# Optimization experiments

Measured on AMD Instinct MI355X. Metric: run time of the kernel, lower is better.

Reference implementation:

```python
import jax, jax.numpy as jnp
import numpy as np

B, T, D = 2, 1024, 1024
NUM_HEADS_ARG = 16
HS = D // NUM_HEADS_ARG          # 64 (per-head size)
H = HS                           # bug in source: num_heads passed = head_size -> 64 heads
FF = 4 * D
EPS = 1e-5


def _layernorm(x, gamma, beta):
    mu = jnp.mean(x, axis=-1, keepdims=True)
    var = jnp.mean(jnp.square(x - mu), axis=-1, keepdims=True)
    return (x - mu) * jax.lax.rsqrt(var + EPS) * gamma + beta


def setup_inputs() -> dict:
    key = jax.random.key(0)
    ks = jax.random.split(key, 12)
    s_d = 1.0 / np.sqrt(D)
    s_cat = 1.0 / np.sqrt(H * HS)
    s_ff = 1.0 / np.sqrt(FF)
    return {
        "x": jax.random.normal(ks[0], (B, T, D), jnp.float32),
        "Wq": jax.random.uniform(ks[1], (H, D, HS), jnp.float32, -s_d, s_d),
        "Wk": jax.random.uniform(ks[2], (H, D, HS), jnp.float32, -s_d, s_d),
        "Wv": jax.random.uniform(ks[3], (H, D, HS), jnp.float32, -s_d, s_d),
        "Wo": jax.random.uniform(ks[4], (H * HS, D), jnp.float32, -s_cat, s_cat),
        "bo": jax.random.uniform(ks[5], (D,), jnp.float32, -s_cat, s_cat),
        "W1": jax.random.uniform(ks[6], (D, FF), jnp.float32, -s_d, s_d),
        "b1": jax.random.uniform(ks[7], (FF,), jnp.float32, -s_d, s_d),
        "W2": jax.random.uniform(ks[8], (FF, D), jnp.float32, -s_ff, s_ff),
        "b2": jax.random.uniform(ks[9], (D,), jnp.float32, -s_ff, s_ff),
        "g1": jnp.ones((D,), jnp.float32),
        "be1": jnp.zeros((D,), jnp.float32),
        "g2": jnp.ones((D,), jnp.float32),
        "be2": jnp.zeros((D,), jnp.float32),
    }


def reference(x, Wq, Wk, Wv, Wo, bo, W1, b1, W2, b2, g1, be1, g2, be2):
    # per-head projections (no bias): [B,H,T,hs]
    q = jnp.einsum('btd,hde->bhte', x, Wq)
    k = jnp.einsum('btd,hde->bhte', x, Wk)
    v = jnp.einsum('btd,hde->bhte', x, Wv)
    scores = jnp.einsum('bhte,bhse->bhts', q, k) / np.sqrt(HS)  # [B,H,T,T]
    causal = jnp.tril(jnp.ones((T, T), bool))
    scores = jnp.where(causal, scores, -jnp.inf)
    probs = jax.nn.softmax(scores, axis=-1)
    att = jnp.einsum('bhts,bhse->bhte', probs, v)               # [B,H,T,hs]
    # torch stack(dim=3) -> [B,T,hs,H] then flatten: index = d*H + h
    cat = jnp.transpose(att, (0, 2, 3, 1)).reshape(B, T, HS * H)
    mha = cat @ Wo + bo
    x1 = _layernorm(x + mha, g1, be1)
    ff = jax.nn.relu(x1 @ W1 + b1) @ W2 + b2
    return _layernorm(x1 + ff, g2, be2)
```

## Files before the change

### kernel.cpp

```cpp
#include <hip/hip_runtime.h>

typedef unsigned short u16;
typedef __bf16 bf16x8 __attribute__((ext_vector_type(8)));
typedef float f32x4 __attribute__((ext_vector_type(4)));

#define B_ 2
#define T_ 1024
#define D_ 1024
#define H_ 64
#define HS_ 64
#define FF_ 4096
#define SZ_QKV 8388608L
#define S_SCALE 0.1803368801111f

__device__ __forceinline__ float bf2f(u16 u) {
  union { unsigned int v; float f; } x; x.v = ((unsigned int)u) << 16; return x.f;
}
__device__ __forceinline__ u16 f2bf(float f) {
  union { float f; unsigned int v; } x; x.f = f;
  unsigned int r = x.v + 0x7fffu + ((x.v >> 16) & 1u);
  return (u16)(r >> 16);
}
__device__ __forceinline__ u16 f2bf_rtz(float f) {
  union { float f; unsigned int v; } x; x.f = f;
  return (u16)(x.v >> 16);
}

typedef __attribute__((address_space(3))) unsigned int lds_u32;
typedef __attribute__((address_space(1))) const unsigned int glb_u32;
__device__ __forceinline__ void gload_lds16(const void* g, void* l) {
  __builtin_amdgcn_global_load_lds((glb_u32*)g, (lds_u32*)l, 16, 0, 0);
}

__global__ __launch_bounds__(256) void prep(
    const float* __restrict__ x, const float* __restrict__ Wq,
    const float* __restrict__ Wk, const float* __restrict__ Wv,
    const float* __restrict__ Wo, const float* __restrict__ W1,
    const float* __restrict__ W2,
    u16* __restrict__ xb, u16* __restrict__ Wqkvt, u16* __restrict__ Wot,
    u16* __restrict__ W1t, u16* __restrict__ W2t)
{
  __shared__ float tile[64][65];
  int id = blockIdx.x;
  if (id < 1024) {
    const long i = ((long)id * 256 + threadIdx.x) * 8;
    float4 a = *(const float4*)(x + i);
    float4 b = *(const float4*)(x + i + 4);
    union { uint4 v; u16 u[8]; } o;
    o.u[0]=f2bf(a.x); o.u[1]=f2bf(a.y); o.u[2]=f2bf(a.z); o.u[3]=f2bf(a.w);
    o.u[4]=f2bf(b.x); o.u[5]=f2bf(b.y); o.u[6]=f2bf(b.z); o.u[7]=f2bf(b.w);
    *(uint4*)(xb + i) = o.v;
    return;
  }
  id -= 1024;
  const float* in; u16* out; long ibase, obase; int in_rs, out_rs, r0, c0;
  if (id < 3072) {
    const int w = id >> 10, rem = id & 1023;
    const int z = rem >> 4, rt = rem & 15;
    in = (w == 0) ? Wq : (w == 1) ? Wk : Wv;
    ibase = (long)z * 65536; in_rs = 64; r0 = rt * 64; c0 = 0;
    out = Wqkvt + (long)w * 4194304;
    obase = (long)z * 65536; out_rs = 1024;
  } else if (id < 4096) {
    const int rem = id - 3072;
    const int z = rem >> 4, ct = rem & 15;
    in = Wo; ibase = (long)z * 1024; in_rs = 65536; r0 = 0; c0 = ct * 64;
    out = Wot; obase = (long)z * 64; out_rs = 4096;
  } else if (id < 5120) {
    const int rem = id - 4096;
    const int rt = rem >> 6, ct = rem & 63;
    in = W1; ibase = 0; in_rs = 4096; r0 = rt * 64; c0 = ct * 64;
    out = W1t; obase = 0; out_rs = 1024;
  } else {
    const int rem = id - 5120;
    const int rt = rem >> 4, ct = rem & 15;
    in = W2; ibase = 0; in_rs = 1024; r0 = rt * 64; c0 = ct * 64;
    out = W2t; obase = 0; out_rs = 4096;
  }
  const int t = threadIdx.x, lr = t >> 4, lc4 = (t & 15) * 4;
  #pragma unroll
  for (int j = 0; j < 4; ++j) {
    float4 f = *(const float4*)(in + ibase + (long)(r0 + lr + j * 16) * in_rs + c0 + lc4);
    tile[lr + j * 16][lc4]     = f.x;
    tile[lr + j * 16][lc4 + 1] = f.y;
    tile[lr + j * 16][lc4 + 2] = f.z;
    tile[lr + j * 16][lc4 + 3] = f.w;
  }
  __syncthreads();
  const int cr = t >> 3, ch = t & 7;
  #pragma unroll
  for (int j2 = 0; j2 < 2; ++j2) {
    const int crr = cr + j2 * 32;
    union { uint4 v; u16 u[8]; } o;
    #pragma unroll
    for (int i = 0; i < 8; ++i) o.u[i] = f2bf(tile[ch * 8 + i][crr]);
    *(uint4*)(out + obase + (long)(c0 + crr) * out_rs + r0 + ch * 8) = o.v;
  }
}

template<int EPI, int LDA, int LDB>
__global__ __launch_bounds__(256, 2) void gemm2(
    const u16* __restrict__ A, const u16* __restrict__ Bt, u16* __restrict__ C,
    const float* __restrict__ bias, int K, int koff, int ldc)
{
  __shared__ __attribute__((aligned(16))) u16 As[3][256 * 32];
  __shared__ __attribute__((aligned(16))) u16 Bs[3][128 * 32];
  const int bm = blockIdx.x, bn = blockIdx.y, bz = blockIdx.z;
  const long ko = (long)bz * koff;
  const int tid = threadIdx.x, wave = tid >> 6, lane = tid & 63;
  const int quad = lane >> 4, l16 = lane & 15;
  const int wm = (wave & 1) * 128;
  const int wn = (wave >> 1) * 64;
  const int srcswz = ((lane & 3) ^ ((lane >> 3) & 3)) * 8;
  const int arr = lane >> 2;
  const int cs8 = (quad ^ ((l16 >> 1) & 3)) * 8;
  const u16* Arow = A + (long)(bm * 256) * LDA + ko + srcswz;
  const u16* Brow = Bt + (long)(bn * 128) * LDB + ko + srcswz;

  f32x4 acc[8][4];
  #pragma unroll
  for (int i = 0; i < 8; ++i)
    #pragma unroll
    for (int j = 0; j < 4; ++j) acc[i][j] = (f32x4){0.f, 0.f, 0.f, 0.f};

  const int nK = K >> 5;

  auto STAGE = [&](int buf, int t) {
    const int k0 = t << 5;
    #pragma unroll
    for (int it = 0; it < 4; ++it) {
      const int i = it * 4 + wave;
      gload_lds16(Arow + (long)(i * 16 + arr) * LDA + k0, (u16*)As[buf] + i * 512);
    }
    #pragma unroll
    for (int it = 0; it < 2; ++it) {
      const int i = it * 4 + wave;
      gload_lds16(Brow + (long)(i * 16 + arr) * LDB + k0, (u16*)Bs[buf] + i * 512);
    }
  };

  STAGE(0, 0);
  STAGE(1, 1);
  int cc = 0, cs = 2;
  for (int t = 0; t < nK; ++t) {
    if (t < nK - 1) asm volatile("s_waitcnt vmcnt(6)" ::: "memory");
    else            asm volatile("s_waitcnt vmcnt(0)" ::: "memory");
    __builtin_amdgcn_sched_barrier(0);
    __builtin_amdgcn_s_barrier();
    __builtin_amdgcn_sched_barrier(0);
    if (t + 2 < nK) STAGE(cs, t + 2);
    const u16* At = As[cc];
    const u16* Bl = Bs[cc];
    bf16x8 a[8], b[4];
    #pragma unroll
    for (int j = 0; j < 4; ++j)
      b[j] = *(const bf16x8*)&Bl[(wn + j * 16 + l16) * 32 + cs8];
    #pragma unroll
    for (int i = 0; i < 8; ++i)
      a[i] = *(const bf16x8*)&At[(wm + i * 16 + l16) * 32 + cs8];
    #pragma unroll
    for (int i = 0; i < 8; ++i)
      #pragma unroll
      for (int j = 0; j < 4; ++j)
        acc[i][j] = __builtin_amdgcn_mfma_f32_16x16x32_bf16(a[i], b[j], acc[i][j], 0, 0, 0);
    cc = (cc == 2) ? 0 : cc + 1;
    cs = (cs == 2) ? 0 : cs + 1;
  }

  #pragma unroll
  for (int j = 0; j < 4; ++j) {
    const int col = bn * 128 + wn + j * 16 + l16;
    const float bval = (EPI == 1) ? bias[col] : 0.f;
    #pragma unroll
    for (int i = 0; i < 8; ++i) {
      #pragma unroll
      for (int r = 0; r < 4; ++r) {
        const int row = bm * 256 + wm + i * 16 + quad * 4 + r;
        float vv = acc[i][j][r] + bval;
        if (EPI == 1) vv = fmaxf(vv, 0.f);
        if (EPI == 2) {
          const int which = col >> 12, rem = col & 4095;
          const int h = rem >> 6, e = rem & 63;
          const int bb = row >> 10, t = row & 1023;
          C[(long)which * SZ_QKV + ((long)((bb << 6) + h)) * 65536L + t * 64 + e] = f2bf(vv);
        } else if (EPI == 3) {
          ((float*)C)[(long)bz * 2097152 + (long)row * ldc + col] = vv;
        } else {
          C[(long)row * ldc + col] = f2bf(vv);
        }
      }
    }
  }
}

__global__ __launch_bounds__(256) void attn_flash(
    const u16* __restrict__ Q, const u16* __restrict__ Kg,
    const u16* __restrict__ V, u16* __restrict__ Om)
{
  __shared__ __attribute__((aligned(16))) u16 Ks[2][64][72];
  __shared__ __attribute__((aligned(16))) u16 Vs[2][64][72];
  __shared__ __attribute__((aligned(16))) u16 QP[4][16][72];
  const int bh = blockIdx.x;
  const int qt = gridDim.y - 1 - blockIdx.y;
  const int b = bh >> 6, h = bh & 63;
  const long base = (long)bh * (T_ * HS_);
  const int tid = threadIdx.x;
  const int wave = tid >> 6, lane = tid & 63, quad = lane >> 4, l16 = lane & 15;
  const int sm = tid >> 2, sc = (tid & 3) * 16;
  const int vswz = (sc >> 4) << 3;

  {
    const int qr = lane >> 3, qe = (lane & 7) * 8;
    #pragma unroll
    for (int j = 0; j < 2; ++j) {
      union { uint4 v; u16 u[8]; } a, o;
      a.v = *(const uint4*)(Q + base + (long)(qt * 64 + wave * 16 + qr + j * 8) * HS_ + qe);
      #pragma unroll
      for (int i = 0; i < 8; ++i) o.u[i] = f2bf(bf2f(a.u[i]) * S_SCALE);
      *(uint4*)&QP[wave][qr + j * 8][qe] = o.v;
    }
  }
  bf16x8 aq0 = *(const bf16x8*)&QP[wave][l16][quad * 8];
  bf16x8 aq1 = *(const bf16x8*)&QP[wave][l16][32 + quad * 8];

  float psum[4] = { 0.f, 0.f, 0.f, 0.f };
  f32x4 oacc[4] = { {0,0,0,0}, {0,0,0,0}, {0,0,0,0}, {0,0,0,0} };

  uint4 kA, kB, vA, vB;
  kA = *(const uint4*)(Kg + base + (long)sm * HS_ + sc);
  kB = *(const uint4*)(Kg + base + (long)sm * HS_ + sc + 8);
  vA = *(const uint4*)(V  + base + (long)sm * HS_ + sc);
  vB = *(const uint4*)(V  + base + (long)sm * HS_ + sc + 8);
  {
    *(uint4*)&Ks[0][sm][sc] = kA; *(uint4*)&Ks[0][sm][sc + 8] = kB;
    union { uint4 v; u16 u[8]; } t0, t1; t0.v = vA; t1.v = vB;
    #pragma unroll
    for (int i = 0; i < 8; ++i) Vs[0][sc + i][sm ^ vswz] = t0.u[i];
    #pragma unroll
    for (int i = 0; i < 8; ++i) Vs[0][sc + 8 + i][sm ^ vswz] = t1.u[i];
  }
  __syncthreads();

  for (int kt = 0; kt <= qt; ++kt) {
    const int cur = kt & 1;
    const bool pf = (kt < qt);
    if (pf) {
      const long nb = base + (long)((kt + 1) * 64 + sm) * HS_ + sc;
      kA = *(const uint4*)(Kg + nb); kB = *(const uint4*)(Kg + nb + 8);
      vA = *(const uint4*)(V  + nb); vB = *(const uint4*)(V  + nb + 8);
    }

    f32x4 sacc[4] = { {0,0,0,0}, {0,0,0,0}, {0,0,0,0}, {0,0,0,0} };
    #pragma unroll
    for (int nt = 0; nt < 4; ++nt) {
      bf16x8 b0 = *(const bf16x8*)&Ks[cur][nt * 16 + l16][quad * 8];
      bf16x8 b1 = *(const bf16x8*)&Ks[cur][nt * 16 + l16][32 + quad * 8];
      sacc[nt] = __builtin_amdgcn_mfma_f32_16x16x32_bf16(aq0, b0, sacc[nt], 0, 0, 0);
      sacc[nt] = __builtin_amdgcn_mfma_f32_16x16x32_bf16(aq1, b1, sacc[nt], 0, 0, 0);
    }

    if (kt == qt) {
      #pragma unroll
      for (int nt = 0; nt < 4; ++nt) {
        const int col = nt * 16 + l16;
        #pragma unroll
        for (int r = 0; r < 4; ++r) {
          const int row = wave * 16 + quad * 4 + r;
          float p = exp2f(sacc[nt][r]);
          p = (col <= row) ? p : 0.f;
          sacc[nt][r] = p; psum[r] += p;
        }
      }
    } else {
      #pragma unroll
      for (int nt = 0; nt < 4; ++nt)
        #pragma unroll
        for (int r = 0; r < 4; ++r) {
          const float p = exp2f(sacc[nt][r]);
          sacc[nt][r] = p; psum[r] += p;
        }
    }

    #pragma unroll
    for (int nt = 0; nt < 4; ++nt)
      #pragma unroll
      for (int r = 0; r < 4; ++r)
        QP[wave][quad * 4 + r][nt * 16 + l16] = f2bf_rtz(sacc[nt][r]);
    bf16x8 p0 = *(const bf16x8*)&QP[wave][l16][quad * 8];
    bf16x8 p1 = *(const bf16x8*)&QP[wave][l16][32 + quad * 8];

    #pragma unroll
    for (int et = 0; et < 4; ++et) {
      const int c0 = ((quad ^ et) * 8);
      bf16x8 b0 = *(const bf16x8*)&Vs[cur][et * 16 + l16][c0];
      bf16x8 b1 = *(const bf16x8*)&Vs[cur][et * 16 + l16][32 + c0];
      oacc[et] = __builtin_amdgcn_mfma_f32_16x16x32_bf16(p0, b0, oacc[et], 0, 0, 0);
      oacc[et] = __builtin_amdgcn_mfma_f32_16x16x32_bf16(p1, b1, oacc[et], 0, 0, 0);
    }

    if (pf) {
      const int nxt = 1 - cur;
      *(uint4*)&Ks[nxt][sm][sc] = kA; *(uint4*)&Ks[nxt][sm][sc + 8] = kB;
      union { uint4 v; u16 u[8]; } t0, t1; t0.v = vA; t1.v = vB;
      #pragma unroll
      for (int i = 0; i < 8; ++i) Vs[nxt][sc + i][sm ^ vswz] = t0.u[i];
      #pragma unroll
      for (int i = 0; i < 8; ++i) Vs[nxt][sc + 8 + i][sm ^ vswz] = t1.u[i];
    }
    __syncthreads();
  }

  #pragma unroll
  for (int off = 1; off < 16; off <<= 1)
    #pragma unroll
    for (int r = 0; r < 4; ++r)
      psum[r] += __shfl_xor(psum[r], off, 64);
  u16 (*Os)[72] = Ks[0];
  #pragma unroll
  for (int r = 0; r < 4; ++r) {
    const float rinv = 1.f / fmaxf(psum[r], 1e-20f);
    const int row = wave * 16 + quad * 4 + r;
    #pragma unroll
    for (int et = 0; et < 4; ++et)
      Os[row][et * 16 + l16] = f2bf(oacc[et][r] * rinv);
  }
  const int orow = wave * 16 + (lane >> 3), oe = (lane & 7) * 8;
  #pragma unroll
  for (int it = 0; it < 2; ++it) {
    const int rr = orow + it * 8;
    uint4 o = *(const uint4*)&Os[rr][oe];
    *(uint4*)(Om + ((long)(b * T_ + qt * 64 + rr)) * 4096 + h * 64 + oe) = o;
  }
}

template<int XBF, int OBF>
__global__ __launch_bounds__(256) void ln_sum4(
    const float* __restrict__ P4, const float* __restrict__ bias,
    const void* __restrict__ Xv, const float* __restrict__ g,
    const float* __restrict__ be, void* __restrict__ outv)
{
  __shared__ float red[8];
  const int row = blockIdx.x, tid = threadIdx.x;
  const long base = (long)row * D_;
  float v4[4]; float s = 0.f;
  #pragma unroll
  for (int j = 0; j < 4; ++j) {
    const int i = tid + j * 256;
    float acc = bias[i];
    #pragma unroll
    for (int p = 0; p < 4; ++p) acc += P4[(long)p * 2097152 + base + i];
    const float xval = XBF ? bf2f(((const u16*)Xv)[base + i]) : ((const float*)Xv)[base + i];
    v4[j] = xval + acc;
    s += v4[j];
  }
  #pragma unroll
  for (int off = 32; off > 0; off >>= 1) s += __shfl_down(s, off, 64);
  if ((tid & 63) == 0) red[tid >> 6] = s;
  __syncthreads();
  const float mu = (red[0] + red[1] + red[2] + red[3]) * (1.f / D_);
  float vs = 0.f;
  #pragma unroll
  for (int j = 0; j < 4; ++j) { const float d = v4[j] - mu; vs += d * d; }
  #pragma unroll
  for (int off = 32; off > 0; off >>= 1) vs += __shfl_down(vs, off, 64);
  __syncthreads();
  if ((tid & 63) == 0) red[tid >> 6] = vs;
  __syncthreads();
  const float rs = rsqrtf((red[0] + red[1] + red[2] + red[3]) * (1.f / D_) + 1e-5f);
  #pragma unroll
  for (int j = 0; j < 4; ++j) {
    const int i = tid + j * 256;
    const float o = (v4[j] - mu) * rs * g[i] + be[i];
    if (OBF) ((u16*)outv)[base + i] = f2bf(o);
    else     ((float*)outv)[base + i] = o;
  }
}

extern "C" void kernel_launch(void* const* d_in, const int* in_sizes, int n_in,
                              void* d_out, int out_size, void* d_ws, size_t ws_size,
                              hipStream_t stream) {
  const float* x   = (const float*)d_in[0];
  const float* Wq  = (const float*)d_in[1];
  const float* Wk  = (const float*)d_in[2];
  const float* Wv  = (const float*)d_in[3];
  const float* Wo  = (const float*)d_in[4];
  const float* bo  = (const float*)d_in[5];
  const float* W1  = (const float*)d_in[6];
  const float* b1  = (const float*)d_in[7];
  const float* W2  = (const float*)d_in[8];
  const float* b2  = (const float*)d_in[9];
  const float* g1  = (const float*)d_in[10];
  const float* be1 = (const float*)d_in[11];
  const float* g2  = (const float*)d_in[12];
  const float* be2 = (const float*)d_in[13];
  float* out = (float*)d_out;

  u16* ws = (u16*)d_ws;
  u16* xb    = ws;
  u16* Wqkvt = xb + 2097152;
  u16* Wot   = Wqkvt + 12582912;
  u16* W1t   = Wot + 4194304;
  u16* W2t   = W1t + 4194304;
  u16* q     = W2t + 4194304;
  u16* k     = q + SZ_QKV;
  u16* v     = k + SZ_QKV;
  u16* Om    = v + SZ_QKV;
  float* P1 = (float*)q;
  float* P2 = (float*)q;
  u16* x1  = v;
  u16* h1  = Om;

  dim3 blk(256);

  prep<<<dim3(7168), blk, 0, stream>>>(x, Wq, Wk, Wv, Wo, W1, W2,
                                       xb, Wqkvt, Wot, W1t, W2t);

  gemm2<2, 1024, 1024><<<dim3(8, 96), blk, 0, stream>>>(
      xb, Wqkvt, q, nullptr, 1024, 0, 0);

  attn_flash<<<dim3(128, 16), blk, 0, stream>>>(q, k, v, Om);

  gemm2<3, 4096, 4096><<<dim3(8, 8, 4), blk, 0, stream>>>(
      Om, Wot, (u16*)P1, nullptr, 1024, 1024, 1024);

  ln_sum4<0, 1><<<dim3(2048), blk, 0, stream>>>(P1, bo, x, g1, be1, x1);

  gemm2<1, 1024, 1024><<<dim3(8, 32), blk, 0, stream>>>(
      x1, W1t, h1, b1, 1024, 0, 4096);

  gemm2<3, 4096, 4096><<<dim3(8, 8, 4), blk, 0, stream>>>(
      h1, W2t, (u16*)P2, nullptr, 1024, 1024, 1024);

  ln_sum4<1, 0><<<dim3(2048), blk, 0, stream>>>(P2, b2, x1, g2, be2, out);

  (void)in_sizes; (void)n_in; (void)out_size; (void)ws_size;
}
```

Before: 405.6 us.

## Replace 4-wave GEMM with 8-wave interleaved load/MFMA pipeline, K-tile 64

Replaces the 256-thread GEMM with a 512-thread kernel in which each of 8 waves computes a 64x64 sub-tile, and the K-step doubles to 64 with an XOR-swizzled LDS layout. Each K iteration is split into four quarter-phases. In each phase, LDS fragment loads and staged global-to-LDS copies for tile t+2 are interleaved with MFMA bursts under s_setprio and barriers, so memory traffic overlaps compute. The three-buffer LDS footprint grows to about 147KB, which allows only one block per CU. The extra barriers per iteration add synchronisation cost.

Result: faster. 387.9 us (-4.4%).

```diff
diff --git a/kernel.cpp b/kernel.cpp
--- a/kernel.cpp
+++ b/kernel.cpp
@@ -99,72 +99,148 @@
 }
 
 template<int EPI, int LDA, int LDB>
-__global__ __launch_bounds__(256, 2) void gemm2(
+__global__ __launch_bounds__(512, 2) void gemm8(
     const u16* __restrict__ A, const u16* __restrict__ Bt, u16* __restrict__ C,
     const float* __restrict__ bias, int K, int koff, int ldc)
 {
-  __shared__ __attribute__((aligned(16))) u16 As[3][256 * 32];
-  __shared__ __attribute__((aligned(16))) u16 Bs[3][128 * 32];
+  __shared__ __attribute__((aligned(16))) u16 As[3][256 * 64];
+  __shared__ __attribute__((aligned(16))) u16 Bs[3][128 * 64];
   const int bm = blockIdx.x, bn = blockIdx.y, bz = blockIdx.z;
   const long ko = (long)bz * koff;
   const int tid = threadIdx.x, wave = tid >> 6, lane = tid & 63;
   const int quad = lane >> 4, l16 = lane & 15;
-  const int wm = (wave & 1) * 128;
-  const int wn = (wave >> 1) * 64;
-  const int srcswz = ((lane & 3) ^ ((lane >> 3) & 3)) * 8;
-  const int arr = lane >> 2;
-  const int cs8 = (quad ^ ((l16 >> 1) & 3)) * 8;
-  const u16* Arow = A + (long)(bm * 256) * LDA + ko + srcswz;
-  const u16* Brow = Bt + (long)(bn * 128) * LDB + ko + srcswz;
-
-  f32x4 acc[8][4];
-  #pragma unroll
-  for (int i = 0; i < 8; ++i)
+  const int wm = (wave >> 1) * 64;
+  const int wn = (wave & 1) * 64;
+  const int slog = ((tid & 7) ^ ((tid >> 3) & 7)) * 8;
+  const int srow = tid >> 3;
+  const int ph0 = ((quad)     ^ (l16 & 7)) * 8;
+  const int ph1 = ((4 + quad) ^ (l16 & 7)) * 8;
+
+  const u16* Ag = A + (long)(bm * 256) * LDA + ko + slog;
+  const u16* Bg = Bt + (long)(bn * 128) * LDB + ko + slog;
+
+  f32x4 acc[4][4];
+  #pragma unroll
+  for (int i = 0; i < 4; ++i)
     #pragma unroll
     for (int j = 0; j < 4; ++j) acc[i][j] = (f32x4){0.f, 0.f, 0.f, 0.f};
 
-  const int nK = K >> 5;
-
-  auto STAGE = [&](int buf, int t) {
-    const int k0 = t << 5;
-    #pragma unroll
-    for (int it = 0; it < 4; ++it) {
-      const int i = it * 4 + wave;
-      gload_lds16(Arow + (long)(i * 16 + arr) * LDA + k0, (u16*)As[buf] + i * 512);
-    }
-    #pragma unroll
-    for (int it = 0; it < 2; ++it) {
-      const int i = it * 4 + wave;
-      gload_lds16(Brow + (long)(i * 16 + arr) * LDB + k0, (u16*)Bs[buf] + i * 512);
-    }
+  const int nK = K >> 6;
+
+  auto STAGE_A = [&](int d, int t, int half) {
+    const int kk = t << 6;
+    gload_lds16(Ag + (long)(half * 128 + srow) * LDA + kk,
+                (u16*)As[d] + (half * 1024 + tid) * 8);
+    gload_lds16(Ag + (long)(half * 128 + 64 + srow) * LDA + kk,
+                (u16*)As[d] + (half * 1024 + 512 + tid) * 8);
   };
-
-  STAGE(0, 0);
-  STAGE(1, 1);
-  int cc = 0, cs = 2;
+  auto STAGE_B = [&](int d, int t) {
+    const int kk = t << 6;
+    gload_lds16(Bg + (long)(srow) * LDB + kk, (u16*)Bs[d] + tid * 8);
+    gload_lds16(Bg + (long)(64 + srow) * LDB + kk, (u16*)Bs[d] + (512 + tid) * 8);
+  };
+
+  STAGE_A(0, 0, 0); STAGE_A(0, 0, 1); STAGE_B(0, 0);
+  STAGE_A(1, 1, 0); STAGE_A(1, 1, 1); STAGE_B(1, 1);
+
+  bf16x8 a0[2][2], b0[2][2], b1[2][2];
+  int cur = 0;
   for (int t = 0; t < nK; ++t) {
-    if (t < nK - 1) asm volatile("s_waitcnt vmcnt(6)" ::: "memory");
-    else            asm volatile("s_waitcnt vmcnt(0)" ::: "memory");
-    __builtin_amdgcn_sched_barrier(0);
-    __builtin_amdgcn_s_barrier();
-    __builtin_amdgcn_sched_barrier(0);
-    if (t + 2 < nK) STAGE(cs, t + 2);
-    const u16* At = As[cc];
-    const u16* Bl = Bs[cc];
-    bf16x8 a[8], b[4];
-    #pragma unroll
-    for (int j = 0; j < 4; ++j)
-      b[j] = *(const bf16x8*)&Bl[(wn + j * 16 + l16) * 32 + cs8];
-    #pragma unroll
-    for (int i = 0; i < 8; ++i)
-      a[i] = *(const bf16x8*)&At[(wm + i * 16 + l16) * 32 + cs8];
-    #pragma unroll
-    for (int i = 0; i < 8; ++i)
-      #pragma unroll
-      for (int j = 0; j < 4; ++j)
-        acc[i][j] = __builtin_amdgcn_mfma_f32_16x16x32_bf16(a[i], b[j], acc[i][j], 0, 0, 0);
-    cc = (cc == 2) ? 0 : cc + 1;
-    cs = (cs == 2) ? 0 : cs + 1;
+    const int nxt = (cur >= 1) ? cur - 1 : cur + 2;
+    const bool st = (t + 2) < nK;
+    const u16* Ab = As[cur];
+    const u16* Bb = Bs[cur];
+
+    if (t < nK - 1) { asm volatile("s_waitcnt vmcnt(6)" ::: "memory"); }
+    else            { asm volatile("s_waitcnt vmcnt(0)" ::: "memory"); }
+    __builtin_amdgcn_sched_barrier(0);
+    __builtin_amdgcn_s_barrier();
+    __builtin_amdgcn_sched_barrier(0);
+    #pragma unroll
+    for (int ii = 0; ii < 2; ++ii) {
+      const u16* r = Ab + (wm + ii * 16 + l16) * 64;
+      a0[ii][0] = *(const bf16x8*)(r + ph0);
+      a0[ii][1] = *(const bf16x8*)(r + ph1);
+    }
+    #pragma unroll
+    for (int jj = 0; jj < 2; ++jj) {
+      const u16* r = Bb + (wn + jj * 16 + l16) * 64;
+      b0[jj][0] = *(const bf16x8*)(r + ph0);
+      b0[jj][1] = *(const bf16x8*)(r + ph1);
+    }
+    asm volatile("s_waitcnt lgkmcnt(0)" ::: "memory");
+    __builtin_amdgcn_sched_barrier(0);
+    __builtin_amdgcn_s_setprio(1);
+    #pragma unroll
+    for (int ii = 0; ii < 2; ++ii)
+      #pragma unroll
+      for (int jj = 0; jj < 2; ++jj) {
+        acc[ii][jj] = __builtin_amdgcn_mfma_f32_16x16x32_bf16(a0[ii][0], b0[jj][0], acc[ii][jj], 0, 0, 0);
+        acc[ii][jj] = __builtin_amdgcn_mfma_f32_16x16x32_bf16(a0[ii][1], b0[jj][1], acc[ii][jj], 0, 0, 0);
+      }
+    __builtin_amdgcn_s_setprio(0);
+    __builtin_amdgcn_sched_barrier(0);
+    __builtin_amdgcn_s_barrier();
+
+    #pragma unroll
+    for (int jj = 0; jj < 2; ++jj) {
+      const u16* r = Bb + (wn + (2 + jj) * 16 + l16) * 64;
+      b1[jj][0] = *(const bf16x8*)(r + ph0);
+      b1[jj][1] = *(const bf16x8*)(r + ph1);
+    }
+    if (st) STAGE_A(nxt, t + 2, 0);
+    __builtin_amdgcn_s_barrier();
+    asm volatile("s_waitcnt lgkmcnt(0)" ::: "memory");
+    __builtin_amdgcn_sched_barrier(0);
+    __builtin_amdgcn_s_setprio(1);
+    #pragma unroll
+    for (int ii = 0; ii < 2; ++ii)
+      #pragma unroll
+      for (int jj = 0; jj < 2; ++jj) {
+        acc[ii][2 + jj] = __builtin_amdgcn_mfma_f32_16x16x32_bf16(a0[ii][0], b1[jj][0], acc[ii][2 + jj], 0, 0, 0);
+        acc[ii][2 + jj] = __builtin_amdgcn_mfma_f32_16x16x32_bf16(a0[ii][1], b1[jj][1], acc[ii][2 + jj], 0, 0, 0);
+      }
+    __builtin_amdgcn_s_setprio(0);
+    __builtin_amdgcn_sched_barrier(0);
+    __builtin_amdgcn_s_barrier();
+
+    #pragma unroll
+    for (int ii = 0; ii < 2; ++ii) {
+      const u16* r = Ab + (wm + (2 + ii) * 16 + l16) * 64;
+      a0[ii][0] = *(const bf16x8*)(r + ph0);
+      a0[ii][1] = *(const bf16x8*)(r + ph1);
+    }
+    if (st) STAGE_A(nxt, t + 2, 1);
+    __builtin_amdgcn_s_barrier();
+    asm volatile("s_waitcnt lgkmcnt(0)" ::: "memory");
+    __builtin_amdgcn_sched_barrier(0);
+    __builtin_amdgcn_s_setprio(1);
+    #pragma unroll
+    for (int ii = 0; ii < 2; ++ii)
+      #pragma unroll
+      for (int jj = 0; jj < 2; ++jj) {
+        acc[2 + ii][jj] = __builtin_amdgcn_mfma_f32_16x16x32_bf16(a0[ii][0], b0[jj][0], acc[2 + ii][jj], 0, 0, 0);
+        acc[2 + ii][jj] = __builtin_amdgcn_mfma_f32_16x16x32_bf16(a0[ii][1], b0[jj][1], acc[2 + ii][jj], 0, 0, 0);
+      }
+    __builtin_amdgcn_s_setprio(0);
+    __builtin_amdgcn_sched_barrier(0);
+    __builtin_amdgcn_s_barrier();
+
+    if (st) STAGE_B(nxt, t + 2);
+    __builtin_amdgcn_s_barrier();
+    __builtin_amdgcn_s_setprio(1);
+    #pragma unroll
+    for (int ii = 0; ii < 2; ++ii)
+      #pragma unroll
+      for (int jj = 0; jj < 2; ++jj) {
+        acc[2 + ii][2 + jj] = __builtin_amdgcn_mfma_f32_16x16x32_bf16(a0[ii][0], b1[jj][0], acc[2 + ii][2 + jj], 0, 0, 0);
+        acc[2 + ii][2 + jj] = __builtin_amdgcn_mfma_f32_16x16x32_bf16(a0[ii][1], b1[jj][1], acc[2 + ii][2 + jj], 0, 0, 0);
+      }
+    __builtin_amdgcn_s_setprio(0);
+    __builtin_amdgcn_sched_barrier(0);
+    __builtin_amdgcn_s_barrier();
+
+    cur = (cur == 2) ? 0 : cur + 1;
   }
 
   #pragma unroll
@@ -172,7 +248,7 @@
     const int col = bn * 128 + wn + j * 16 + l16;
     const float bval = (EPI == 1) ? bias[col] : 0.f;
     #pragma unroll
-    for (int i = 0; i < 8; ++i) {
+    for (int i = 0; i < 4; ++i) {
       #pragma unroll
       for (int r = 0; r < 4; ++r) {
         const int row = bm * 256 + wm + i * 16 + quad * 4 + r;
@@ -181,8 +257,8 @@
         if (EPI == 2) {
           const int which = col >> 12, rem = col & 4095;
           const int h = rem >> 6, e = rem & 63;
-          const int bb = row >> 10, t = row & 1023;
-          C[(long)which * SZ_QKV + ((long)((bb << 6) + h)) * 65536L + t * 64 + e] = f2bf(vv);
+          const int bb = row >> 10, tt = row & 1023;
+          C[(long)which * SZ_QKV + ((long)((bb << 6) + h)) * 65536L + tt * 64 + e] = f2bf(vv);
         } else if (EPI == 3) {
           ((float*)C)[(long)bz * 2097152 + (long)row * ldc + col] = vv;
         } else {
@@ -411,24 +487,25 @@
   u16* h1  = Om;
 
   dim3 blk(256);
+  dim3 blk8(512);
 
   prep<<<dim3(7168), blk, 0, stream>>>(x, Wq, Wk, Wv, Wo, W1, W2,
                                        xb, Wqkvt, Wot, W1t, W2t);
 
-  gemm2<2, 1024, 1024><<<dim3(8, 96), blk, 0, stream>>>(
+  gemm8<2, 1024, 1024><<<dim3(8, 96), blk8, 0, stream>>>(
       xb, Wqkvt, q, nullptr, 1024, 0, 0);
 
   attn_flash<<<dim3(128, 16), blk, 0, stream>>>(q, k, v, Om);
 
-  gemm2<3, 4096, 4096><<<dim3(8, 8, 4), blk, 0, stream>>>(
+  gemm8<3, 4096, 4096><<<dim3(8, 8, 4), blk8, 0, stream>>>(
       Om, Wot, (u16*)P1, nullptr, 1024, 1024, 1024);
 
   ln_sum4<0, 1><<<dim3(2048), blk, 0, stream>>>(P1, bo, x, g1, be1, x1);
 
-  gemm2<1, 1024, 1024><<<dim3(8, 32), blk, 0, stream>>>(
+  gemm8<1, 1024, 1024><<<dim3(8, 32), blk8, 0, stream>>>(
       x1, W1t, h1, b1, 1024, 0, 4096);
 
-  gemm2<3, 4096, 4096><<<dim3(8, 8, 4), blk, 0, stream>>>(
+  gemm8<3, 4096, 4096><<<dim3(8, 8, 4), blk8, 0, stream>>>(
       h1, W2t, (u16*)P2, nullptr, 1024, 1024, 1024);
 
   ln_sum4<1, 0><<<dim3(2048), blk, 0, stream>>>(P2, b2, x1, g2, be2, out);
```
